# Kernel optimization log

Measured on AMD Instinct MI355X. Metric: run time of the kernel, lower is better.

The kernel has to match this reference:

```python
import jax, jax.numpy as jnp
import numpy as np

SOFTEN = 10000.0
COLOR_NORM = 1.0
COLOR_JITTER = 0.0
EPS = 1e-8


def setup_inputs() -> dict:
    key = jax.random.key(0)
    k1, k2, k3, k4, k5 = jax.random.split(key, 5)
    B, C, H, W = 4, 64, 512, 512
    K, HID = 16, 128
    img = jax.random.uniform(k1, (B, 3, H, W), dtype=jnp.float32)
    feat = jax.random.normal(k2, (B, C, H, W), dtype=jnp.float32)
    W1 = jax.random.normal(k3, (HID, C), dtype=jnp.float32) * 0.05
    b1 = jax.random.normal(k4, (HID,), dtype=jnp.float32) * 0.05
    W2 = jax.random.normal(k5, (K, HID), dtype=jnp.float32) * 0.05
    return {"img": img, "feat": feat, "W1": W1, "b1": b1, "W2": W2, "training": 0}


def reference(img, feat, W1, b1, W2, training):
    # color_mask head: two 1x1 convs (pure channel contractions)
    h = jax.nn.relu(jnp.einsum('bchw,oc->bohw', feat, W1) + b1[None, :, None, None])
    logits = jnp.einsum('bohw,ko->bkhw', h, W2)           # [B,K,H,W]
    m = jax.nn.softmax(SOFTEN * logits, axis=1)           # Softmax2d over channel dim
    K = m.shape[1]
    M = jnp.argmax(m, axis=1)                             # [B,H,W]
    # one-hot indicator, channel-first: [B,K,H,W]
    indicator = (jnp.arange(K)[None, :, None, None] == M[:, None]).astype(m.dtype)
    if training:
        w = m
        norm = COLOR_NORM
    else:
        w = indicator
        norm = 1.0
    # weighted spatial reduction instead of materializing [B,K,3,H,W]
    num = jnp.einsum('bkhw,bchw->bkc', w, img)            # [B,K,3]
    den = jnp.sum(w, axis=(2, 3))                         # [B,K]
    palette = num / (den[:, :, None] + EPS) / norm        # [B,K,3]
    if training:
        palette_used = palette + COLOR_JITTER * np.random.randn()
    else:
        palette_used = palette
    transformed_img = jnp.einsum('bkhw,bkc->bchw', w, palette_used)  # [B,3,H,W]
    color_palette = palette[:, :, :, None, None]          # keepdim [B,K,3,1,1]
    return transformed_img, m, color_palette
```

## Files before the change

kernel.cpp:

```cpp
#include <hip/hip_runtime.h>

#define HW_  262144
#define C_   64
#define HID_ 128
#define K_   16
#define B_   4
#define NPIX (B_*HW_)

typedef __attribute__((ext_vector_type(8)))  short bf16x8;
typedef __attribute__((ext_vector_type(16))) float f32x16;
typedef __attribute__((ext_vector_type(4)))  short short4v;

#define W1F_BYTE 2048
#define W2F_BYTE 34816
#define LBL_BYTE 51200
#define WS_NEED_FAST ((size_t)LBL_BYTE + (size_t)NPIX*4)

__device__ __forceinline__ unsigned short f2bf(float x) {
    unsigned u = __float_as_uint(x);
    unsigned r = u + 0x7FFFu + ((u >> 16) & 1u);
    return (unsigned short)(r >> 16);
}
__device__ __forceinline__ float bf2f(unsigned short h) {
    return __uint_as_float(((unsigned)h) << 16);
}
__device__ __forceinline__ f32x16 mfma32(bf16x8 a, bf16x8 b, f32x16 c) {
    return __builtin_amdgcn_mfma_f32_32x32x16_bf16(a, b, c, 0, 0, 0);
}


__global__ __launch_bounds__(256) void prep_fast(
    const float* __restrict__ W1, const float* __restrict__ W2,
    float* __restrict__ wsf)
{
    int gi = blockIdx.x*256 + threadIdx.x;
    if (gi < 256) wsf[gi] = 0.0f;
    unsigned short* w1f = (unsigned short*)((char*)wsf + W1F_BYTE);
    unsigned short* w2f = (unsigned short*)((char*)wsf + W2F_BYTE);
    if (gi < 8192) {
        int j = gi & 7, l = (gi >> 3) & 63, s = (gi >> 9) & 3, m = (gi >> 11) & 3;
        int o = 32*m + (l & 31);
        int c = 16*s + 8*(l >> 5) + j;
        float w  = W1[o*C_ + c];
        unsigned short hi = f2bf(w);
        unsigned short lo = f2bf(w - bf2f(hi));
        int base = ((m*4 + s)*2)*512 + l*8 + j;
        w1f[base]       = hi;
        w1f[base + 512] = lo;
    } else if (gi < 12288) {
        int i = gi - 8192;
        int j = i & 7, l = (i >> 3) & 63, t = (i >> 9) & 7;
        int k = l & 31;
        int o = 16*t + 8*(l >> 5) + j;
        float w = (k < K_) ? W2[k*HID_ + o] : 0.0f;
        unsigned short hi = f2bf(w);
        unsigned short lo = f2bf(w - bf2f(hi));
        int base = (t*2)*512 + l*8 + j;
        w2f[base]       = hi;
        w2f[base + 512] = lo;
    }
}

__global__ __launch_bounds__(256, 2) void mlp_mfma(
    const float* __restrict__ feat, const float* __restrict__ img,
    const float* __restrict__ b1,
    const unsigned short* __restrict__ w1f, const unsigned short* __restrict__ w2f,
    float* __restrict__ m_out, float* __restrict__ accum, int* __restrict__ labels)
{
    __shared__ float b1s[HID_];
    __shared__ float bins[K_*4];
    __shared__ short hhi[4][32][72];
    __shared__ short hlo[4][32][72];

    int t = threadIdx.x, lane = t & 63, w = t >> 6;
    int col = lane & 31, half = lane >> 5;
    if (t < HID_) b1s[t] = b1[t];
    if (t < K_*4) bins[t] = 0.0f;
    __syncthreads();

    int blk = blockIdx.x;
    int b   = blk >> 11;
    int px0 = (blk & 2047)*128 + w*32;
    int px  = px0 + col;
    const float* fb = feat + ((size_t)b*C_ << 18) + px;

    f32x16 acc[4];
#pragma unroll
    for (int m = 0; m < 4; ++m) acc[m] = 0.0f;

    const bf16x8* w1v = (const bf16x8*)w1f;
#pragma unroll
    for (int s = 0; s < 4; ++s) {
        int c0 = 16*s + 8*half;
        float fv[8];
#pragma unroll
        for (int j = 0; j < 8; ++j)
            fv[j] = fb[(size_t)(c0 + j) << 18];
        bf16x8 bh, bl;
#pragma unroll
        for (int j = 0; j < 8; ++j) {
            unsigned short hi = f2bf(fv[j]);
            bh[j] = (short)hi;
            bl[j] = (short)f2bf(fv[j] - bf2f(hi));
        }
#pragma unroll
        for (int m = 0; m < 4; ++m) {
            const bf16x8* p = w1v + ((m*4 + s)*2)*64 + lane;
            bf16x8 ah = p[0];
            bf16x8 al = p[64];
            acc[m] = mfma32(ah, bh, acc[m]);
            acc[m] = mfma32(al, bh, acc[m]);
            acc[m] = mfma32(ah, bl, acc[m]);
        }
    }

    f32x16 acc2 = 0.0f;
    const bf16x8* w2v = (const bf16x8*)w2f;
#pragma unroll
    for (int chunk = 0; chunk < 2; ++chunk) {
#pragma unroll
        for (int ml = 0; ml < 2; ++ml) {
            int m = chunk*2 + ml;
#pragma unroll
            for (int q = 0; q < 4; ++q) {
                short4v vh, vl;
#pragma unroll
                for (int i = 0; i < 4; ++i) {
                    int r = q*4 + i;
                    int o = 32*m + 8*q + 4*half + i;
                    float hval = fmaxf(acc[m][r] + b1s[o], 0.0f);
                    unsigned short hi = f2bf(hval);
                    vh[i] = (short)hi;
                    vl[i] = (short)f2bf(hval - bf2f(hi));
                }
                int ob = 32*ml + 8*q + 4*half;
                *(short4v*)&hhi[w][col][ob] = vh;
                *(short4v*)&hlo[w][col][ob] = vl;
            }
        }
#pragma unroll
        for (int tt = 0; tt < 4; ++tt) {
            int tg = chunk*4 + tt;
            bf16x8 bh2 = *(const bf16x8*)&hhi[w][col][tt*16 + 8*half];
            bf16x8 bl2 = *(const bf16x8*)&hlo[w][col][tt*16 + 8*half];
            const bf16x8* p = w2v + (tg*2)*64 + lane;
            bf16x8 ah = p[0];
            bf16x8 al = p[64];
            acc2 = mfma32(ah, bh2, acc2);
            acc2 = mfma32(al, bh2, acc2);
            acc2 = mfma32(ah, bl2, acc2);
        }
    }

    float lg[8]; int kk[8];
#pragma unroll
    for (int r = 0; r < 8; ++r) {
        lg[r] = acc2[r];
        kk[r] = (r & 3) + 8*(r >> 2) + 4*half;
    }
    float mx = lg[0]; int ki = kk[0];
#pragma unroll
    for (int r = 1; r < 8; ++r)
        if (lg[r] > mx) { mx = lg[r]; ki = kk[r]; }
    float mxo = __shfl_xor(mx, 32);
    int   kio = __shfl_xor(ki, 32);
    if (mxo > mx || (mxo == mx && kio < ki)) { mx = mxo; ki = kio; }

    float es[8], ss = 0.0f;
#pragma unroll
    for (int r = 0; r < 8; ++r) {
        es[r] = __expf(1.0e4f * (lg[r] - mx));
        ss += es[r];
    }
    ss += __shfl_xor(ss, 32);
    float inv = 1.0f / ss;

    size_t mbase = (size_t)(b*K_) << 18;
#pragma unroll
    for (int r = 0; r < 8; ++r)
        m_out[mbase + ((size_t)kk[r] << 18) + px] = es[r] * inv;

    if (half == 0) {
        labels[((size_t)b << 18) + px] = ki;
        const float* ip = img + ((size_t)(b*3) << 18) + px;
        atomicAdd(&bins[ki*4+0], ip[0]);
        atomicAdd(&bins[ki*4+1], ip[(size_t)1 << 18]);
        atomicAdd(&bins[ki*4+2], ip[(size_t)2 << 18]);
        atomicAdd(&bins[ki*4+3], 1.0f);
    }
    __syncthreads();
    if (t < K_*4) atomicAdd(&accum[b*K_*4 + t], bins[t]);
}

__global__ __launch_bounds__(64) void palette_kernel(
    const float* __restrict__ accum, float* __restrict__ pal_out,
    float* __restrict__ palf)
{
    int t = threadIdx.x;
    float den  = accum[t*4+3];
    float invd = 1.0f / (den + 1e-8f);
#pragma unroll
    for (int c = 0; c < 3; ++c) {
        float pal = accum[t*4+c] * invd;
        palf[t*3+c]    = pal;
        pal_out[t*3+c] = pal;
    }
}

__global__ __launch_bounds__(256) void recolor_lbl_kernel(
    const int* __restrict__ labels, const float* __restrict__ palf,
    float* __restrict__ timg)
{
    int g = blockIdx.x*256 + threadIdx.x;
    int b = g >> 18;
    int p = g & (HW_-1);
    int ks = labels[g];
#pragma unroll
    for (int c = 0; c < 3; ++c)
        timg[((size_t)(b*3+c) << 18) + p] = palf[(b*K_ + ks)*3 + c];
}


__global__ __launch_bounds__(256) void prep_scalar(
    const float* __restrict__ W1, const float* __restrict__ b1,
    const float* __restrict__ W2, float* __restrict__ wsf)
{
    int t = threadIdx.x;
    wsf[t] = 0.0f;
    for (int i = t; i < HID_*C_; i += 256) wsf[256 + i] = W1[i];
    if (t < HID_) wsf[8448 + t] = b1[t];
    for (int i = t; i < K_*HID_; i += 256) {
        int k = i / HID_, o = i % HID_;
        wsf[8576 + o*K_ + k] = W2[i];
    }
}

__global__ __launch_bounds__(256) void mlp_scalar(
    const float* __restrict__ feat, const float* __restrict__ img,
    const float* __restrict__ wsf, float* __restrict__ m_out,
    float* __restrict__ accum)
{
    __shared__ float bins[K_*4];
    int t = threadIdx.x;
    if (t < K_*4) bins[t] = 0.0f;
    __syncthreads();
    int g = blockIdx.x*256 + t;
    int b = g >> 18, p = g & (HW_-1);
    const float* fp = feat + ((size_t)(b*C_) << 18) + p;
    float f[C_];
#pragma unroll
    for (int c = 0; c < C_; ++c) f[c] = fp[(size_t)c << 18];
    const float* W1f = wsf + 256;
    const float* b1f = wsf + 8448;
    const float* W2T = wsf + 8576;
    float logits[K_];
#pragma unroll
    for (int k = 0; k < K_; ++k) logits[k] = 0.0f;
    for (int o = 0; o < HID_; ++o) {
        float h = b1f[o];
#pragma unroll
        for (int c = 0; c < C_; ++c) h = fmaf(f[c], W1f[o*C_ + c], h);
        h = fmaxf(h, 0.0f);
#pragma unroll
        for (int k = 0; k < K_; ++k) logits[k] = fmaf(h, W2T[o*K_ + k], logits[k]);
    }
    float lmax = logits[0]; int kstar = 0;
#pragma unroll
    for (int k = 1; k < K_; ++k)
        if (logits[k] > lmax) { lmax = logits[k]; kstar = k; }
    float ex[K_], esum = 0.0f;
#pragma unroll
    for (int k = 0; k < K_; ++k) { ex[k] = __expf(1.0e4f*(logits[k]-lmax)); esum += ex[k]; }
    float inv = 1.0f / esum;
#pragma unroll
    for (int k = 0; k < K_; ++k)
        m_out[((size_t)(b*K_ + k) << 18) + p] = ex[k] * inv;
    const float* ip = img + ((size_t)(b*3) << 18) + p;
    atomicAdd(&bins[kstar*4+0], ip[0]);
    atomicAdd(&bins[kstar*4+1], ip[(size_t)1 << 18]);
    atomicAdd(&bins[kstar*4+2], ip[(size_t)2 << 18]);
    atomicAdd(&bins[kstar*4+3], 1.0f);
    __syncthreads();
    if (t < K_*4) atomicAdd(&accum[b*K_*4 + t], bins[t]);
}

__global__ __launch_bounds__(256) void recolor_m_kernel(
    const float* __restrict__ m_in, const float* __restrict__ palf,
    float* __restrict__ timg)
{
    int g = blockIdx.x*256 + threadIdx.x;
    int b = g >> 18, p = g & (HW_-1);
    const float* mp = m_in + ((size_t)(b*K_) << 18) + p;
    float best = -1.0f; int ks = 0;
#pragma unroll
    for (int k = 0; k < K_; ++k) {
        float v = mp[(size_t)k << 18];
        if (v > best) { best = v; ks = k; }
    }
#pragma unroll
    for (int c = 0; c < 3; ++c)
        timg[((size_t)(b*3+c) << 18) + p] = palf[(b*K_ + ks)*3 + c];
}

extern "C" void kernel_launch(void* const* d_in, const int* in_sizes, int n_in,
                              void* d_out, int out_size, void* d_ws, size_t ws_size,
                              hipStream_t stream)
{
    const float* img  = (const float*)d_in[0];
    const float* feat = (const float*)d_in[1];
    const float* W1   = (const float*)d_in[2];
    const float* b1   = (const float*)d_in[3];
    const float* W2   = (const float*)d_in[4];

    float* out0 = (float*)d_out;
    float* out1 = out0 + (size_t)B_*3*HW_;
    float* out2 = out1 + (size_t)B_*K_*HW_;
    float* wsf  = (float*)d_ws;

    if (ws_size >= WS_NEED_FAST) {
        const unsigned short* w1f = (const unsigned short*)((char*)d_ws + W1F_BYTE);
        const unsigned short* w2f = (const unsigned short*)((char*)d_ws + W2F_BYTE);
        int* lbl = (int*)((char*)d_ws + LBL_BYTE);
        float* palf = wsf + 256;
        prep_fast<<<48, 256, 0, stream>>>(W1, W2, wsf);
        mlp_mfma<<<NPIX/128, 256, 0, stream>>>(feat, img, b1,
                                               w1f, w2f, out1, wsf, lbl);
        palette_kernel<<<1, 64, 0, stream>>>(wsf, out2, palf);
        recolor_lbl_kernel<<<NPIX/256, 256, 0, stream>>>(lbl, palf, out0);
    } else {
        prep_scalar<<<1, 256, 0, stream>>>(W1, b1, W2, wsf);
        mlp_scalar<<<NPIX/256, 256, 0, stream>>>(feat, img, wsf, out1, wsf);
        palette_kernel<<<1, 64, 0, stream>>>(wsf, out2, wsf + 10624);
        recolor_m_kernel<<<NPIX/256, 256, 0, stream>>>(out1, wsf + 10624, out0);
    }
}
```

Measured before the change: 533.4 us.

## Hoist all feature loads and pass hidden activations via lane shuffles

All 32 feature loads per lane are issued up front before any MFMA work, which exposes more memory-level parallelism. The hidden activations going into the second MFMA used to be staged through shared memory. They are now packed as hi/lo bf16 pairs and swapped between lane halves with __shfl_xor, which removes the LDS buffers. Launch bounds rise from 2 to 3 blocks per SM to raise occupancy, at the risk of register pressure or spills, since 32 floats plus the bf16 arrays are now live together.

```diff
diff --git a/kernel.cpp b/kernel.cpp
--- a/kernel.cpp
+++ b/kernel.cpp
@@ -9,7 +9,6 @@
 
 typedef __attribute__((ext_vector_type(8)))  short bf16x8;
 typedef __attribute__((ext_vector_type(16))) float f32x16;
-typedef __attribute__((ext_vector_type(4)))  short short4v;
 
 #define W1F_BYTE 2048
 #define W2F_BYTE 34816
@@ -61,7 +60,7 @@
     }
 }
 
-__global__ __launch_bounds__(256, 2) void mlp_mfma(
+__global__ __launch_bounds__(256, 3) void mlp_mfma(
     const float* __restrict__ feat, const float* __restrict__ img,
     const float* __restrict__ b1,
     const unsigned short* __restrict__ w1f, const unsigned short* __restrict__ w2f,
@@ -69,8 +68,6 @@
 {
     __shared__ float b1s[HID_];
     __shared__ float bins[K_*4];
-    __shared__ short hhi[4][32][72];
-    __shared__ short hlo[4][32][72];
 
     int t = threadIdx.x, lane = t & 63, w = t >> 6;
     int col = lane & 31, half = lane >> 5;
@@ -80,76 +77,78 @@
 
     int blk = blockIdx.x;
     int b   = blk >> 11;
-    int px0 = (blk & 2047)*128 + w*32;
-    int px  = px0 + col;
+    int px  = (blk & 2047)*128 + w*32 + col;
     const float* fb = feat + ((size_t)b*C_ << 18) + px;
 
+    float fv[32];
+#pragma unroll
+    for (int s = 0; s < 4; ++s)
+#pragma unroll
+        for (int j = 0; j < 8; ++j)
+            fv[s*8 + j] = fb[(size_t)(16*s + 8*half + j) << 18];
+
+    bf16x8 bh[4], bl[4];
+#pragma unroll
+    for (int s = 0; s < 4; ++s)
+#pragma unroll
+        for (int j = 0; j < 8; ++j) {
+            float x = fv[s*8 + j];
+            unsigned short hi = f2bf(x);
+            bh[s][j] = (short)hi;
+            bl[s][j] = (short)f2bf(x - bf2f(hi));
+        }
+
     f32x16 acc[4];
 #pragma unroll
     for (int m = 0; m < 4; ++m) acc[m] = 0.0f;
 
     const bf16x8* w1v = (const bf16x8*)w1f;
 #pragma unroll
-    for (int s = 0; s < 4; ++s) {
-        int c0 = 16*s + 8*half;
-        float fv[8];
-#pragma unroll
-        for (int j = 0; j < 8; ++j)
-            fv[j] = fb[(size_t)(c0 + j) << 18];
-        bf16x8 bh, bl;
-#pragma unroll
-        for (int j = 0; j < 8; ++j) {
-            unsigned short hi = f2bf(fv[j]);
-            bh[j] = (short)hi;
-            bl[j] = (short)f2bf(fv[j] - bf2f(hi));
-        }
+    for (int s = 0; s < 4; ++s)
 #pragma unroll
         for (int m = 0; m < 4; ++m) {
             const bf16x8* p = w1v + ((m*4 + s)*2)*64 + lane;
             bf16x8 ah = p[0];
             bf16x8 al = p[64];
-            acc[m] = mfma32(ah, bh, acc[m]);
-            acc[m] = mfma32(al, bh, acc[m]);
-            acc[m] = mfma32(ah, bl, acc[m]);
+            acc[m] = mfma32(ah, bh[s], acc[m]);
+            acc[m] = mfma32(al, bh[s], acc[m]);
+            acc[m] = mfma32(ah, bl[s], acc[m]);
         }
-    }
 
     f32x16 acc2 = 0.0f;
     const bf16x8* w2v = (const bf16x8*)w2f;
 #pragma unroll
-    for (int chunk = 0; chunk < 2; ++chunk) {
-#pragma unroll
-        for (int ml = 0; ml < 2; ++ml) {
-            int m = chunk*2 + ml;
-#pragma unroll
-            for (int q = 0; q < 4; ++q) {
-                short4v vh, vl;
-#pragma unroll
-                for (int i = 0; i < 4; ++i) {
-                    int r = q*4 + i;
-                    int o = 32*m + 8*q + 4*half + i;
-                    float hval = fmaxf(acc[m][r] + b1s[o], 0.0f);
-                    unsigned short hi = f2bf(hval);
-                    vh[i] = (short)hi;
-                    vl[i] = (short)f2bf(hval - bf2f(hi));
-                }
-                int ob = 32*ml + 8*q + 4*half;
-                *(short4v*)&hhi[w][col][ob] = vh;
-                *(short4v*)&hlo[w][col][ob] = vl;
-            }
+    for (int tg = 0; tg < 8; ++tg) {
+        int m = tg >> 1, sub = tg & 1;
+        unsigned pk[8];
+#pragma unroll
+        for (int i = 0; i < 8; ++i) {
+            int r = 8*sub + i;
+            int o = 32*m + (i & 3) + 16*sub + 8*(i >> 2) + 4*half;
+            float hv = fmaxf(acc[m][r] + b1s[o], 0.0f);
+            unsigned short hi = f2bf(hv);
+            unsigned short lo = f2bf(hv - bf2f(hi));
+            pk[i] = ((unsigned)hi) | (((unsigned)lo) << 16);
         }
-#pragma unroll
-        for (int tt = 0; tt < 4; ++tt) {
-            int tg = chunk*4 + tt;
-            bf16x8 bh2 = *(const bf16x8*)&hhi[w][col][tt*16 + 8*half];
-            bf16x8 bl2 = *(const bf16x8*)&hlo[w][col][tt*16 + 8*half];
-            const bf16x8* p = w2v + (tg*2)*64 + lane;
-            bf16x8 ah = p[0];
-            bf16x8 al = p[64];
-            acc2 = mfma32(ah, bh2, acc2);
-            acc2 = mfma32(al, bh2, acc2);
-            acc2 = mfma32(ah, bl2, acc2);
+        bf16x8 bh2, bl2;
+#pragma unroll
+        for (int j = 0; j < 4; ++j) {
+            unsigned ov = half ? pk[j+4] : pk[j];
+            unsigned sv = half ? pk[j]   : pk[j+4];
+            unsigned rv = (unsigned)__shfl_xor((int)sv, 32);
+            unsigned lowsrc  = half ? rv : ov;
+            unsigned highsrc = half ? ov : rv;
+            bh2[j]   = (short)(lowsrc  & 0xffffu);
+            bl2[j]   = (short)(lowsrc  >> 16);
+            bh2[j+4] = (short)(highsrc & 0xffffu);
+            bl2[j+4] = (short)(highsrc >> 16);
         }
+        const bf16x8* p = w2v + (tg*2)*64 + lane;
+        bf16x8 ah = p[0];
+        bf16x8 al = p[64];
+        acc2 = mfma32(ah, bh2, acc2);
+        acc2 = mfma32(al, bh2, acc2);
+        acc2 = mfma32(ah, bl2, acc2);
     }
 
     float lg[8]; int kk[8];
@@ -219,7 +218,6 @@
     for (int c = 0; c < 3; ++c)
         timg[((size_t)(b*3+c) << 18) + p] = palf[(b*K_ + ks)*3 + c];
 }
-
 
 __global__ __launch_bounds__(256) void prep_scalar(
     const float* __restrict__ W1, const float* __restrict__ b1,
```

Result: faster. 514.5 us (-3.5%).
